# Kernel optimization log

Measured on AMD Instinct MI355X. Metric: run time of the kernel, lower is better.

The kernel has to match this reference:

```python
import jax, jax.numpy as jnp
import numpy as np

B, L = 4, 1024
D_IN, D_MODEL = 2, 512
N_LAYERS, D_STATE, D_CONV, EXPAND, DT_RANK = 2, 16, 4, 2, 32
D_INNER = EXPAND * D_MODEL
EPS = 1e-5


def setup_inputs() -> dict:
    key = jax.random.key(0)
    ks = jax.random.split(key, 10)
    s = 0.02
    return {
        "x": jax.random.normal(ks[0], (B, L, D_IN), jnp.float32),
        "emb_W": jax.random.normal(ks[1], (D_MODEL, D_IN), jnp.float32) * s,
        "emb_b": jnp.zeros((D_MODEL,), jnp.float32),
        "norm_w": jnp.ones((N_LAYERS, D_MODEL), jnp.float32),
        "in_proj_W": jax.random.normal(ks[2], (N_LAYERS, 2 * D_INNER, D_MODEL), jnp.float32) * s,
        "conv_W": jax.random.normal(ks[3], (N_LAYERS, D_INNER, 1, D_CONV), jnp.float32) * s,
        "conv_b": jnp.zeros((N_LAYERS, D_INNER), jnp.float32),
        "x_proj_W": jax.random.normal(ks[4], (N_LAYERS, DT_RANK + 2 * D_STATE, D_INNER), jnp.float32) * s,
        "dt_proj_W": jax.random.normal(ks[5], (N_LAYERS, D_INNER, DT_RANK), jnp.float32) * s,
        "dt_proj_b": jax.random.uniform(ks[6], (N_LAYERS, D_INNER), jnp.float32, -4.0, -2.0),
        "A_log": jnp.log(jnp.broadcast_to(jnp.arange(1, D_STATE + 1, dtype=jnp.float32), (N_LAYERS, D_INNER, D_STATE)) + 0.0),
        "Dskip": jnp.ones((N_LAYERS, D_INNER), jnp.float32),
        "out_proj_W": jax.random.normal(ks[7], (N_LAYERS, D_MODEL, D_INNER), jnp.float32) * s,
        "normf_w": jnp.ones((D_MODEL,), jnp.float32),
    }


def rmsnorm(x, w):
    return x * jax.lax.rsqrt(jnp.mean(x * x, axis=-1, keepdims=True) + EPS) * w


def selective_scan(u, delta, A, Bm, Cm, Dskip):
    # u, delta: (B,L,ED); A: (ED,N); Bm, Cm: (B,L,N); Dskip: (ED,)
    deltaA = jnp.exp(delta[..., None] * A)                      # (B,L,ED,N)
    BX = (delta[..., None] * Bm[:, :, None, :]) * u[..., None]  # (B,L,ED,N)

    def step(h, inp):
        dA, bx, c = inp
        h = dA * h + bx                       # (B,ED,N)
        y = jnp.einsum('ben,bn->be', h, c)    # (B,ED)
        return h, y

    h0 = jnp.zeros((u.shape[0], u.shape[2], A.shape[1]), u.dtype)
    _, ys = jax.lax.scan(step, h0, (deltaA.swapaxes(0, 1), BX.swapaxes(0, 1), Cm.swapaxes(0, 1)))
    y = ys.swapaxes(0, 1)                     # (B,L,ED)
    return y + Dskip * u


def mamba_layer(x, norm_w, ipW, cW, cb, xpW, dtW, dtb, A_log, Dk, opW):
    h = rmsnorm(x, norm_w)
    xz = h @ ipW.T                            # (B,L,2*ED)
    u, z = jnp.split(xz, 2, axis=-1)
    # causal depthwise conv over sequence dim
    uc = jax.lax.conv_general_dilated(
        u.swapaxes(1, 2), cW, window_strides=(1,), padding=[(D_CONV - 1, 0)],
        feature_group_count=D_INNER, dimension_numbers=('NCH', 'OIH', 'NCH'))
    u = jax.nn.silu(uc.swapaxes(1, 2) + cb)   # (B,L,ED)
    xdb = u @ xpW.T                           # (B,L,dt_rank+2N)
    dt, Bm, Cm = jnp.split(xdb, [DT_RANK, DT_RANK + D_STATE], axis=-1)
    delta = jax.nn.softplus(dt @ dtW.T + dtb)
    A = -jnp.exp(A_log)
    y = selective_scan(u, delta, A, Bm, Cm, Dk)
    y = y * jax.nn.silu(z)
    return x + y @ opW.T


def reference(x, emb_W, emb_b, norm_w, in_proj_W, conv_W, conv_b, x_proj_W,
              dt_proj_W, dt_proj_b, A_log, Dskip, out_proj_W, normf_w):
    h = x @ emb_W.T + emb_b                   # (B,L,D_MODEL)
    for l in range(N_LAYERS):
        h = mamba_layer(h, norm_w[l], in_proj_W[l], conv_W[l], conv_b[l],
                        x_proj_W[l], dt_proj_W[l], dt_proj_b[l], A_log[l],
                        Dskip[l], out_proj_W[l])
    return rmsnorm(h, normf_w)
```

## Files before the change

### kernel.cpp

```cpp
#include <hip/hip_runtime.h>
#include <math.h>
#include <stddef.h>

#define BB 4
#define LL 1024
#define DM 512
#define ED 1024
#define NST 16
#define DTR 32
#define XDBC 64
#define BL (BB*LL)
#define CS 16
#define NC 64
#define XKS 16
#define XPAD 68
#define DPAD 132

typedef __attribute__((ext_vector_type(8))) short bf16x8;
typedef __attribute__((ext_vector_type(4))) float f32x4;
typedef unsigned short ushort_t;

__device__ __forceinline__ float silu_f(float x) { return x / (1.f + __expf(-x)); }

__device__ __forceinline__ ushort_t f2b(float f) {
    unsigned int u = __float_as_uint(f);
    unsigned int r = (u + 0x7FFFu + ((u >> 16) & 1u)) >> 16;
    return (ushort_t)r;
}
__device__ __forceinline__ float b2f(ushort_t v) {
    return __uint_as_float(((unsigned int)v) << 16);
}
__device__ __forceinline__ ushort_t f2h(float f) {
    _Float16 h = (_Float16)f;
    return *(ushort_t*)&h;
}
__device__ __forceinline__ float h2f(ushort_t v) {
    _Float16 h = *(_Float16*)&v;
    return (float)h;
}

__device__ __forceinline__ void gload16(const ushort_t* g, ushort_t* l) {
    __builtin_amdgcn_global_load_lds(
        (const __attribute__((address_space(1))) unsigned int*)g,
        (__attribute__((address_space(3))) unsigned int*)l, 16, 0, 0);
}

__global__ void k_embed(const float* __restrict__ x, const float* __restrict__ W,
                        const float* __restrict__ bias, float* __restrict__ h) {
    int i = blockIdx.x * 256 + threadIdx.x;
    if (i >= BL * DM) return;
    int d = i % DM, r = i / DM;
    h[i] = x[r * 2 + 0] * W[d * 2 + 0] + x[r * 2 + 1] * W[d * 2 + 1] + bias[d];
}

__global__ void k_cvt2(const float* __restrict__ ip, const float* __restrict__ op,
                       ushort_t* __restrict__ wip, ushort_t* __restrict__ wop,
                       int n1, int n2) {
    int i = blockIdx.x * 256 + threadIdx.x;
    const float* src; ushort_t* dst; int q;
    if (i < n1) { src = ip; dst = wip; q = i; }
    else if (i < n1 + n2) { src = op; dst = wop; q = i - n1; }
    else return;
    float4 v = *(const float4*)(src + (size_t)q * 4);
    ushort_t o[4] = {f2b(v.x), f2b(v.y), f2b(v.z), f2b(v.w)};
    *(uint2*)(dst + (size_t)q * 4) = *(uint2*)o;
}

template <int BF16OUT>
__global__ __launch_bounds__(256) void k_rmsnorm(const float* __restrict__ in,
                                                 const float* __restrict__ w,
                                                 void* __restrict__ outp) {
    int m = blockIdx.x;
    int tid = threadIdx.x;
    const float* row = in + (size_t)m * DM;
    float2 v = *(const float2*)(row + tid * 2);
    float ss = v.x * v.x + v.y * v.y;
    #pragma unroll
    for (int o = 32; o > 0; o >>= 1) ss += __shfl_down(ss, o, 64);
    __shared__ float red[4];
    int wid = tid >> 6;
    if ((tid & 63) == 0) red[wid] = ss;
    __syncthreads();
    float tot = red[0] + red[1] + red[2] + red[3];
    float rs = rsqrtf(tot * (1.f / DM) + 1e-5f);
    float2 wv = *(const float2*)(w + tid * 2);
    float ox = v.x * rs * wv.x;
    float oy = v.y * rs * wv.y;
    if (BF16OUT) {
        ushort_t o[2] = {f2b(ox), f2b(oy)};
        *(unsigned int*)((ushort_t*)outp + (size_t)m * DM + tid * 2) = *(unsigned int*)o;
    } else {
        *(float2*)((float*)outp + (size_t)m * DM + tid * 2) = make_float2(ox, oy);
    }
}

template <int ADDRES, int BF16OUT, int NT>
__global__ __launch_bounds__(256) void k_bgemm(const ushort_t* __restrict__ A,
                                               const ushort_t* __restrict__ W,
                                               const float* __restrict__ Res,
                                               void* __restrict__ C,
                                               int M, int N, int K, int lda, int ldc) {
    __shared__ ushort_t As[128 * 32];
    __shared__ ushort_t Bs[NT * 32];
    constexpr int NFJ = NT / 32;
    int tid = threadIdx.x;
    int bm = blockIdx.y * 128, bn = blockIdx.x * NT;
    int wave = tid >> 6, lane = tid & 63;
    int wr = wave >> 1, wc = wave & 1;
    int lr = lane & 15;
    int kc = lane >> 4;
    f32x4 acc[4][NFJ];
    #pragma unroll
    for (int i = 0; i < 4; ++i)
        #pragma unroll
        for (int j = 0; j < NFJ; ++j) acc[i][j] = (f32x4){0.f, 0.f, 0.f, 0.f};

    for (int k0 = 0; k0 < K; k0 += 32) {
        __syncthreads();
        #pragma unroll
        for (int ii = 0; ii < 2; ++ii) {
            int g = wave * 128 + ii * 64 + lane;
            int row = g >> 2;
            int c = (g & 3) ^ ((g >> 3) & 3);
            gload16(A + (size_t)(bm + row) * lda + k0 + c * 8,
                    As + (size_t)(wave * 128 + ii * 64) * 8);
        }
        #pragma unroll
        for (int ii = 0; ii < NFJ / 2; ++ii) {
            int g = wave * (NFJ / 2) * 64 + ii * 64 + lane;
            int row = g >> 2;
            int c = (g & 3) ^ ((g >> 3) & 3);
            gload16(W + (size_t)(bn + row) * K + k0 + c * 8,
                    Bs + (size_t)(wave * (NFJ / 2) * 64 + ii * 64) * 8);
        }
        __syncthreads();
        bf16x8 af[4], bfr[NFJ];
        #pragma unroll
        for (int i = 0; i < 4; ++i) {
            int ra = wr * 64 + i * 16 + lr;
            int ca = kc ^ ((ra >> 1) & 3);
            af[i] = *(const bf16x8*)(As + ra * 32 + ca * 8);
        }
        #pragma unroll
        for (int j = 0; j < NFJ; ++j) {
            int rb = wc * (NT / 2) + j * 16 + lr;
            int cb = kc ^ ((rb >> 1) & 3);
            bfr[j] = *(const bf16x8*)(Bs + rb * 32 + cb * 8);
        }
        #pragma unroll
        for (int i = 0; i < 4; ++i)
            #pragma unroll
            for (int j = 0; j < NFJ; ++j)
                acc[i][j] = __builtin_amdgcn_mfma_f32_16x16x32_bf16(af[i], bfr[j], acc[i][j], 0, 0, 0);
    }
    int crow0 = bm + wr * 64 + (lane >> 4) * 4;
    #pragma unroll
    for (int i = 0; i < 4; ++i)
        #pragma unroll
        for (int j = 0; j < NFJ; ++j)
            #pragma unroll
            for (int r = 0; r < 4; ++r) {
                size_t off = (size_t)(crow0 + i * 16 + r) * ldc + bn + wc * (NT / 2) + j * 16 + lr;
                float v = acc[i][j][r];
                if (ADDRES) v += Res[off];
                if (BF16OUT) ((ushort_t*)C)[off] = f2b(v);
                else         ((float*)C)[off] = v;
            }
}

__global__ __launch_bounds__(256) void k_xproj(const ushort_t* __restrict__ A,
                                               const float* __restrict__ W,
                                               float* __restrict__ Pp) {
    __shared__ float As[64][XPAD];
    __shared__ float Ws[64][XPAD];
    int tid = threadIdx.x;
    int k0 = blockIdx.x * 64;
    int bm = blockIdx.y * 64;
    int r = tid >> 2;
    int kc = (tid & 3) * 16;
    const ushort_t* ap = A + (size_t)(bm + r) * ED + k0 + kc;
    const float4* wp = (const float4*)(W + (size_t)r * ED + k0 + kc);
    uint4 a0 = *(const uint4*)(ap);
    uint4 a1 = *(const uint4*)(ap + 8);
    const ushort_t* pa0 = (const ushort_t*)&a0;
    const ushort_t* pa1 = (const ushort_t*)&a1;
    #pragma unroll
    for (int i = 0; i < 8; ++i) {
        As[kc + i][r] = b2f(pa0[i]);
        As[kc + 8 + i][r] = b2f(pa1[i]);
    }
    #pragma unroll
    for (int i = 0; i < 4; ++i) {
        float4 wv = wp[i];
        Ws[kc + i * 4 + 0][r] = wv.x; Ws[kc + i * 4 + 1][r] = wv.y;
        Ws[kc + i * 4 + 2][r] = wv.z; Ws[kc + i * 4 + 3][r] = wv.w;
    }
    __syncthreads();
    int tm = (tid >> 4) * 4;
    int tn = (tid & 15) * 4;
    float acc[4][4] = {};
    #pragma unroll 4
    for (int k = 0; k < 64; ++k) {
        float4 a = *(const float4*)&As[k][tm];
        float4 b = *(const float4*)&Ws[k][tn];
        acc[0][0] += a.x * b.x; acc[0][1] += a.x * b.y; acc[0][2] += a.x * b.z; acc[0][3] += a.x * b.w;
        acc[1][0] += a.y * b.x; acc[1][1] += a.y * b.y; acc[1][2] += a.y * b.z; acc[1][3] += a.y * b.w;
        acc[2][0] += a.z * b.x; acc[2][1] += a.z * b.y; acc[2][2] += a.z * b.z; acc[2][3] += a.z * b.w;
        acc[3][0] += a.w * b.x; acc[3][1] += a.w * b.y; acc[3][2] += a.w * b.z; acc[3][3] += a.w * b.w;
    }
    float* pp = Pp + (size_t)blockIdx.x * BL * XDBC;
    #pragma unroll
    for (int i = 0; i < 4; ++i)
        *(float4*)(pp + (size_t)(bm + tm + i) * XDBC + tn) =
            make_float4(acc[i][0], acc[i][1], acc[i][2], acc[i][3]);
}

__global__ void k_xred(const float* __restrict__ Pp, float* __restrict__ xdb) {
    int i = blockIdx.x * 256 + threadIdx.x;
    float4 s = make_float4(0.f, 0.f, 0.f, 0.f);
    #pragma unroll
    for (int sl = 0; sl < XKS; ++sl) {
        float4 v = *(const float4*)(Pp + (size_t)sl * BL * XDBC + (size_t)i * 4);
        s.x += v.x; s.y += v.y; s.z += v.z; s.w += v.w;
    }
    *(float4*)(xdb + (size_t)i * 4) = s;
}

__global__ void k_conv(const ushort_t* __restrict__ xzb, const float* __restrict__ cw,
                       const float* __restrict__ cb, ushort_t* __restrict__ u) {
    int i = blockIdx.x * 256 + threadIdx.x;
    if (i >= BL * ED) return;
    int e = i % ED;
    int t = (i / ED) % LL;
    int b = i / (ED * LL);
    const ushort_t* col = xzb + (size_t)b * LL * 2048 + e;
    float4 w4 = *(const float4*)(cw + e * 4);
    float acc = cb[e];
    if (t >= 3) acc += b2f(col[(size_t)(t - 3) * 2048]) * w4.x;
    if (t >= 2) acc += b2f(col[(size_t)(t - 2) * 2048]) * w4.y;
    if (t >= 1) acc += b2f(col[(size_t)(t - 1) * 2048]) * w4.z;
    acc += b2f(col[(size_t)t * 2048]) * w4.w;
    u[i] = f2b(silu_f(acc));
}

__global__ __launch_bounds__(256) void k_delta(const float* __restrict__ xdb,
                                               const float* __restrict__ dtW,
                                               const float* __restrict__ dtb,
                                               ushort_t* __restrict__ dyh) {
    __shared__ float Dt[32][DPAD];
    __shared__ float Wt[32][DPAD];
    int tid = threadIdx.x;
    int bm = blockIdx.y * 128;
    int bn = blockIdx.x * 128;
    int r = tid >> 1;
    int hh = (tid & 1) * 16;
    const float4* dp = (const float4*)(xdb + (size_t)(bm + r) * XDBC + hh);
    const float4* wp = (const float4*)(dtW + (size_t)(bn + r) * 32 + hh);
    #pragma unroll
    for (int i = 0; i < 4; ++i) {
        float4 v = dp[i];
        Dt[hh + i * 4 + 0][r] = v.x; Dt[hh + i * 4 + 1][r] = v.y;
        Dt[hh + i * 4 + 2][r] = v.z; Dt[hh + i * 4 + 3][r] = v.w;
        float4 w = wp[i];
        Wt[hh + i * 4 + 0][r] = w.x; Wt[hh + i * 4 + 1][r] = w.y;
        Wt[hh + i * 4 + 2][r] = w.z; Wt[hh + i * 4 + 3][r] = w.w;
    }
    __syncthreads();
    int tm = (tid >> 4) * 8;
    int tn = (tid & 15) * 8;
    float acc[8][8] = {};
    #pragma unroll 8
    for (int k = 0; k < 32; ++k) {
        float4 a0 = *(const float4*)&Dt[k][tm];
        float4 a1 = *(const float4*)&Dt[k][tm + 4];
        float4 b0 = *(const float4*)&Wt[k][tn];
        float4 b1 = *(const float4*)&Wt[k][tn + 4];
        float a[8] = {a0.x, a0.y, a0.z, a0.w, a1.x, a1.y, a1.z, a1.w};
        float b[8] = {b0.x, b0.y, b0.z, b0.w, b1.x, b1.y, b1.z, b1.w};
        #pragma unroll
        for (int i = 0; i < 8; ++i)
            #pragma unroll
            for (int j = 0; j < 8; ++j) acc[i][j] += a[i] * b[j];
    }
    float4 t0 = *(const float4*)(dtb + bn + tn);
    float4 t1 = *(const float4*)(dtb + bn + tn + 4);
    float bias[8] = {t0.x, t0.y, t0.z, t0.w, t1.x, t1.y, t1.z, t1.w};
    #pragma unroll
    for (int i = 0; i < 8; ++i) {
        ushort_t o16[8];
        #pragma unroll
        for (int j = 0; j < 8; ++j) {
            float v = acc[i][j] + bias[j];
            v = (v > 20.f) ? v : __logf(1.f + __expf(v));
            o16[j] = f2h(v);
        }
        size_t off = (size_t)(bm + tm + i) * ED + bn + tn;
        *(uint4*)(dyh + off) = *(uint4*)o16;
    }
}

__global__ __launch_bounds__(256) void k_scan1(const ushort_t* __restrict__ dyh,
                                               const ushort_t* __restrict__ u,
                                               const float* __restrict__ xdb,
                                               const float* __restrict__ A_log,
                                               float* __restrict__ P,
                                               float* __restrict__ S) {
    int tid = threadIdx.x;
    int e = ((blockIdx.x & 3) << 8) + tid;
    int c = (blockIdx.x >> 2) & (NC - 1);
    int b = blockIdx.x >> 8;
    float Ac[16];
    const float4* ap = (const float4*)(A_log + (size_t)e * NST);
    #pragma unroll
    for (int q = 0; q < 4; ++q) {
        float4 a = ap[q];
        Ac[q * 4 + 0] = -__expf(a.x); Ac[q * 4 + 1] = -__expf(a.y);
        Ac[q * 4 + 2] = -__expf(a.z); Ac[q * 4 + 3] = -__expf(a.w);
    }
    float h[16] = {};
    float s = 0.f;
    const ushort_t* dp = dyh + ((size_t)b * LL + c * CS) * ED + e;
    const ushort_t* up = u + ((size_t)b * LL + c * CS) * ED + e;
    const float* xp = xdb + ((size_t)b * LL + c * CS) * XDBC;
    for (int tt = 0; tt < CS; ++tt) {
        float dv = h2f(dp[(size_t)tt * ED]);
        float uv = b2f(up[(size_t)tt * ED]);
        s += dv;
        float du = dv * uv;
        const float4* bp = (const float4*)(xp + tt * XDBC + DTR);
        #pragma unroll
        for (int q = 0; q < 4; ++q) {
            float4 bv = bp[q];
            h[q * 4 + 0] = __expf(dv * Ac[q * 4 + 0]) * h[q * 4 + 0] + du * bv.x;
            h[q * 4 + 1] = __expf(dv * Ac[q * 4 + 1]) * h[q * 4 + 1] + du * bv.y;
            h[q * 4 + 2] = __expf(dv * Ac[q * 4 + 2]) * h[q * 4 + 2] + du * bv.z;
            h[q * 4 + 3] = __expf(dv * Ac[q * 4 + 3]) * h[q * 4 + 3] + du * bv.w;
        }
    }
    float4* pp = (float4*)(P + ((size_t)(b * NC + c) * ED + e) * NST);
    pp[0] = make_float4(h[0], h[1], h[2], h[3]);
    pp[1] = make_float4(h[4], h[5], h[6], h[7]);
    pp[2] = make_float4(h[8], h[9], h[10], h[11]);
    pp[3] = make_float4(h[12], h[13], h[14], h[15]);
    S[(size_t)(b * NC + c) * ED + e] = s;
}

__global__ __launch_bounds__(256) void k_scan2(float* __restrict__ P,
                                               const float* __restrict__ S,
                                               const float* __restrict__ A_log) {
    int i = blockIdx.x * 256 + threadIdx.x;
    int n = i & 15;
    int e = (i >> 4) & (ED - 1);
    int b = i >> 14;
    float Ac = -__expf(A_log[(size_t)e * NST + n]);
    float hin = 0.f;
    for (int c = 0; c < NC; ++c) {
        size_t base = (size_t)(b * NC + c) * ED + e;
        float p = P[base * NST + n];
        float s = S[base];
        P[base * NST + n] = hin;
        hin = __expf(Ac * s) * hin + p;
    }
}

__global__ __launch_bounds__(256) void k_scan3(const ushort_t* __restrict__ dyh,
                                               const ushort_t* __restrict__ u,
                                               const float* __restrict__ xdb,
                                               const ushort_t* __restrict__ xzb,
                                               const float* __restrict__ A_log,
                                               const float* __restrict__ Dskip,
                                               const float* __restrict__ P,
                                               ushort_t* __restrict__ yb) {
    int tid = threadIdx.x;
    int e = ((blockIdx.x & 3) << 8) + tid;
    int c = (blockIdx.x >> 2) & (NC - 1);
    int b = blockIdx.x >> 8;
    float Ac[16], h[16];
    const float4* ap = (const float4*)(A_log + (size_t)e * NST);
    #pragma unroll
    for (int q = 0; q < 4; ++q) {
        float4 a = ap[q];
        Ac[q * 4 + 0] = -__expf(a.x); Ac[q * 4 + 1] = -__expf(a.y);
        Ac[q * 4 + 2] = -__expf(a.z); Ac[q * 4 + 3] = -__expf(a.w);
    }
    const float4* pp = (const float4*)(P + ((size_t)(b * NC + c) * ED + e) * NST);
    #pragma unroll
    for (int q = 0; q < 4; ++q) {
        float4 hv = pp[q];
        h[q * 4 + 0] = hv.x; h[q * 4 + 1] = hv.y;
        h[q * 4 + 2] = hv.z; h[q * 4 + 3] = hv.w;
    }
    float Dk = Dskip[e];
    const ushort_t* dp = dyh + ((size_t)b * LL + c * CS) * ED + e;
    const ushort_t* up = u + ((size_t)b * LL + c * CS) * ED + e;
    const float* xp = xdb + ((size_t)b * LL + c * CS) * XDBC;
    const ushort_t* zp = xzb + ((size_t)b * LL + c * CS) * 2048 + 1024 + e;
    ushort_t* yp = yb + ((size_t)b * LL + c * CS) * ED + e;
    for (int tt = 0; tt < CS; ++tt) {
        float dv = h2f(dp[(size_t)tt * ED]);
        float uv = b2f(up[(size_t)tt * ED]);
        float zv = b2f(zp[(size_t)tt * 2048]);
        float du = dv * uv;
        const float4* bp = (const float4*)(xp + tt * XDBC + DTR);
        const float4* cp = (const float4*)(xp + tt * XDBC + DTR + NST);
        float y = 0.f;
        #pragma unroll
        for (int q = 0; q < 4; ++q) {
            float4 bv = bp[q];
            float4 cv = cp[q];
            h[q * 4 + 0] = __expf(dv * Ac[q * 4 + 0]) * h[q * 4 + 0] + du * bv.x;
            h[q * 4 + 1] = __expf(dv * Ac[q * 4 + 1]) * h[q * 4 + 1] + du * bv.y;
            h[q * 4 + 2] = __expf(dv * Ac[q * 4 + 2]) * h[q * 4 + 2] + du * bv.z;
            h[q * 4 + 3] = __expf(dv * Ac[q * 4 + 3]) * h[q * 4 + 3] + du * bv.w;
            y += h[q * 4 + 0] * cv.x + h[q * 4 + 1] * cv.y +
                 h[q * 4 + 2] * cv.z + h[q * 4 + 3] * cv.w;
        }
        yp[(size_t)tt * ED] = f2b((y + Dk * uv) * silu_f(zv));
    }
}

extern "C" void kernel_launch(void* const* d_in, const int* in_sizes, int n_in,
                              void* d_out, int out_size, void* d_ws, size_t ws_size,
                              hipStream_t stream) {
    const float* x     = (const float*)d_in[0];
    const float* embW  = (const float*)d_in[1];
    const float* embB  = (const float*)d_in[2];
    const float* normw = (const float*)d_in[3];
    const float* ipW   = (const float*)d_in[4];
    const float* cW    = (const float*)d_in[5];
    const float* cb    = (const float*)d_in[6];
    const float* xpW   = (const float*)d_in[7];
    const float* dtW   = (const float*)d_in[8];
    const float* dtb   = (const float*)d_in[9];
    const float* Alog  = (const float*)d_in[10];
    const float* Dsk   = (const float*)d_in[11];
    const float* opW   = (const float*)d_in[12];
    const float* normfw= (const float*)d_in[13];
    float* out = (float*)d_out;

    float* ws  = (float*)d_ws;
    float* h   = ws;
    ushort_t* xzb = (ushort_t*)(h + (size_t)BL * DM);
    ushort_t* ub  = xzb + (size_t)BL * 2 * ED;
    float* xdb = (float*)(ub + (size_t)BL * ED);
    float* Pp  = xdb + (size_t)BL * XDBC;
    float* S   = Pp + (size_t)XKS * BL * XDBC;
    ushort_t* wip = (ushort_t*)(S + (size_t)BB * NC * ED);
    ushort_t* wop = wip + (size_t)2 * 2 * ED * DM;
    ushort_t* yb  = wop + (size_t)2 * DM * ED;
    float* P      = Pp;
    ushort_t* hnb = (ushort_t*)d_out;
    ushort_t* dyh = (ushort_t*)d_out;

    k_embed<<<(BL * DM + 255) / 256, 256, 0, stream>>>(x, embW, embB, h);
    int n1 = 2 * 2 * ED * DM / 4, n2 = 2 * DM * ED / 4;
    k_cvt2<<<(n1 + n2 + 255) / 256, 256, 0, stream>>>(ipW, opW, wip, wop, n1, n2);

    for (int l = 0; l < 2; ++l) {
        const float* Al = Alog + (size_t)l * ED * NST;
        k_rmsnorm<1><<<BL, 256, 0, stream>>>(h, normw + (size_t)l * DM, hnb);
        k_bgemm<0, 1, 128><<<dim3(2 * ED / 128, BL / 128), 256, 0, stream>>>(
            hnb, wip + (size_t)l * 2 * ED * DM, nullptr, xzb, BL, 2 * ED, DM, DM, 2 * ED);
        k_conv<<<(BL * ED + 255) / 256, 256, 0, stream>>>(
            xzb, cW + (size_t)l * ED * 4, cb + (size_t)l * ED, ub);
        k_xproj<<<dim3(XKS, BL / 64), 256, 0, stream>>>(
            ub, xpW + (size_t)l * XDBC * ED, Pp);
        k_xred<<<BL * XDBC / 4 / 256, 256, 0, stream>>>(Pp, xdb);
        k_delta<<<dim3(ED / 128, BL / 128), 256, 0, stream>>>(
            xdb, dtW + (size_t)l * ED * DTR, dtb + (size_t)l * ED, dyh);
        k_scan1<<<BB * NC * (ED / 256), 256, 0, stream>>>(dyh, ub, xdb, Al, P, S);
        k_scan2<<<BB * ED * NST / 256, 256, 0, stream>>>(P, S, Al);
        k_scan3<<<BB * NC * (ED / 256), 256, 0, stream>>>(
            dyh, ub, xdb, xzb, Al, Dsk + (size_t)l * ED, P, yb);
        k_bgemm<1, 0, 64><<<dim3(DM / 64, BL / 128), 256, 0, stream>>>(
            yb, wop + (size_t)l * DM * ED, h, h, BL, DM, ED, ED, DM);
    }
    k_rmsnorm<0><<<BL, 256, 0, stream>>>(h, normfw, out);
}
```

Measured before the change: 297.3 us.

## Fuse conv, x_proj, and dt_proj into one row-tiled mid kernel

Replaces the separate causal-conv, split-K x_proj, reduction, and delta kernels with a single kernel. Each block handles 16 rows: it computes conv+SiLU into shared memory, does the full-K x_proj with a two-way K split reduced in shared memory, then computes dt_proj+softplus from the shared xdb tile. Embedding and weight conversion are also merged into one launch. This removes three launches and the split-K partial buffer round trip. In exchange it uses a scalar FMA GEMM with reloaded x_proj weights per block and only 256 blocks, which may limit parallelism.

```diff
diff --git a/kernel.cpp b/kernel.cpp
--- a/kernel.cpp
+++ b/kernel.cpp
@@ -12,9 +12,7 @@
 #define BL (BB*LL)
 #define CS 16
 #define NC 64
-#define XKS 16
-#define XPAD 68
-#define DPAD 132
+#define MT 16
 
 typedef __attribute__((ext_vector_type(8))) short bf16x8;
 typedef __attribute__((ext_vector_type(4))) float f32x4;
@@ -45,21 +43,21 @@
         (__attribute__((address_space(3))) unsigned int*)l, 16, 0, 0);
 }
 
-__global__ void k_embed(const float* __restrict__ x, const float* __restrict__ W,
-                        const float* __restrict__ bias, float* __restrict__ h) {
+__global__ void k_init(const float* __restrict__ x, const float* __restrict__ embW,
+                       const float* __restrict__ embB, float* __restrict__ h,
+                       const float* __restrict__ ipW, const float* __restrict__ opW,
+                       ushort_t* __restrict__ wip, ushort_t* __restrict__ wop,
+                       int nEmb, int n1, int n2) {
     int i = blockIdx.x * 256 + threadIdx.x;
-    if (i >= BL * DM) return;
-    int d = i % DM, r = i / DM;
-    h[i] = x[r * 2 + 0] * W[d * 2 + 0] + x[r * 2 + 1] * W[d * 2 + 1] + bias[d];
-}
-
-__global__ void k_cvt2(const float* __restrict__ ip, const float* __restrict__ op,
-                       ushort_t* __restrict__ wip, ushort_t* __restrict__ wop,
-                       int n1, int n2) {
-    int i = blockIdx.x * 256 + threadIdx.x;
+    if (i < nEmb) {
+        int d = i % DM, r = i / DM;
+        h[i] = x[r * 2 + 0] * embW[d * 2 + 0] + x[r * 2 + 1] * embW[d * 2 + 1] + embB[d];
+        return;
+    }
+    i -= nEmb;
     const float* src; ushort_t* dst; int q;
-    if (i < n1) { src = ip; dst = wip; q = i; }
-    else if (i < n1 + n2) { src = op; dst = wop; q = i - n1; }
+    if (i < n1) { src = ipW; dst = wip; q = i; }
+    else if (i < n1 + n2) { src = opW; dst = wop; q = i - n1; }
     else return;
     float4 v = *(const float4*)(src + (size_t)q * 4);
     ushort_t o[4] = {f2b(v.x), f2b(v.y), f2b(v.z), f2b(v.w)};
@@ -168,134 +166,122 @@
             }
 }
 
-__global__ __launch_bounds__(256) void k_xproj(const ushort_t* __restrict__ A,
-                                               const float* __restrict__ W,
-                                               float* __restrict__ Pp) {
-    __shared__ float As[64][XPAD];
-    __shared__ float Ws[64][XPAD];
+__global__ __launch_bounds__(512) void k_mid(const ushort_t* __restrict__ xzb,
+                                             const float* __restrict__ cw,
+                                             const float* __restrict__ cb,
+                                             const float* __restrict__ xpW,
+                                             const float* __restrict__ dtW,
+                                             const float* __restrict__ dtb,
+                                             ushort_t* __restrict__ ub,
+                                             float* __restrict__ xdb,
+                                             ushort_t* __restrict__ dyh) {
+    __shared__ ushort_t Ut[MT][1032];
+    __shared__ float Wt[64][68];
+    __shared__ float Xs[MT][68];
+    __shared__ float Xs2[MT][68];
     int tid = threadIdx.x;
-    int k0 = blockIdx.x * 64;
-    int bm = blockIdx.y * 64;
-    int r = tid >> 2;
-    int kc = (tid & 3) * 16;
-    const ushort_t* ap = A + (size_t)(bm + r) * ED + k0 + kc;
-    const float4* wp = (const float4*)(W + (size_t)r * ED + k0 + kc);
-    uint4 a0 = *(const uint4*)(ap);
-    uint4 a1 = *(const uint4*)(ap + 8);
-    const ushort_t* pa0 = (const ushort_t*)&a0;
-    const ushort_t* pa1 = (const ushort_t*)&a1;
-    #pragma unroll
-    for (int i = 0; i < 8; ++i) {
-        As[kc + i][r] = b2f(pa0[i]);
-        As[kc + 8 + i][r] = b2f(pa1[i]);
-    }
-    #pragma unroll
-    for (int i = 0; i < 4; ++i) {
-        float4 wv = wp[i];
-        Ws[kc + i * 4 + 0][r] = wv.x; Ws[kc + i * 4 + 1][r] = wv.y;
-        Ws[kc + i * 4 + 2][r] = wv.z; Ws[kc + i * 4 + 3][r] = wv.w;
+    int bm = blockIdx.x * MT;
+
+    {
+        int e0 = (tid & 255) * 4;
+        int th = (tid >> 8) * 8;
+        float cw4[4][4], cb4[4];
+        #pragma unroll
+        for (int i = 0; i < 4; ++i) {
+            float4 w = *(const float4*)(cw + (size_t)(e0 + i) * 4);
+            cw4[i][0] = w.x; cw4[i][1] = w.y; cw4[i][2] = w.z; cw4[i][3] = w.w;
+        }
+        float4 cbv = *(const float4*)(cb + e0);
+        cb4[0] = cbv.x; cb4[1] = cbv.y; cb4[2] = cbv.z; cb4[3] = cbv.w;
+        #pragma unroll
+        for (int i = 0; i < 8; ++i) {
+            int t = th + i;
+            int row = bm + t;
+            int tloc = row & (LL - 1);
+            const ushort_t* xrow = xzb + (size_t)row * 2048 + e0;
+            uint2 z2 = make_uint2(0, 0);
+            uint2 v3 = *(const uint2*)xrow;
+            uint2 v2 = (tloc >= 1) ? *(const uint2*)(xrow - 2048) : z2;
+            uint2 v1 = (tloc >= 2) ? *(const uint2*)(xrow - 4096) : z2;
+            uint2 v0 = (tloc >= 3) ? *(const uint2*)(xrow - 6144) : z2;
+            const ushort_t* p0 = (const ushort_t*)&v0;
+            const ushort_t* p1 = (const ushort_t*)&v1;
+            const ushort_t* p2 = (const ushort_t*)&v2;
+            const ushort_t* p3 = (const ushort_t*)&v3;
+            ushort_t ures[4];
+            #pragma unroll
+            for (int e = 0; e < 4; ++e) {
+                float a = cb4[e] + b2f(p0[e]) * cw4[e][0] + b2f(p1[e]) * cw4[e][1]
+                                 + b2f(p2[e]) * cw4[e][2] + b2f(p3[e]) * cw4[e][3];
+                ures[e] = f2b(silu_f(a));
+            }
+            *(uint2*)(&Ut[t][e0]) = *(uint2*)ures;
+            *(uint2*)(ub + (size_t)row * ED + e0) = *(uint2*)ures;
+        }
     }
     __syncthreads();
-    int tm = (tid >> 4) * 4;
-    int tn = (tid & 15) * 4;
-    float acc[4][4] = {};
-    #pragma unroll 4
-    for (int k = 0; k < 64; ++k) {
-        float4 a = *(const float4*)&As[k][tm];
-        float4 b = *(const float4*)&Ws[k][tn];
-        acc[0][0] += a.x * b.x; acc[0][1] += a.x * b.y; acc[0][2] += a.x * b.z; acc[0][3] += a.x * b.w;
-        acc[1][0] += a.y * b.x; acc[1][1] += a.y * b.y; acc[1][2] += a.y * b.z; acc[1][3] += a.y * b.w;
-        acc[2][0] += a.z * b.x; acc[2][1] += a.z * b.y; acc[2][2] += a.z * b.z; acc[2][3] += a.z * b.w;
-        acc[3][0] += a.w * b.x; acc[3][1] += a.w * b.y; acc[3][2] += a.w * b.z; acc[3][3] += a.w * b.w;
-    }
-    float* pp = Pp + (size_t)blockIdx.x * BL * XDBC;
-    #pragma unroll
-    for (int i = 0; i < 4; ++i)
-        *(float4*)(pp + (size_t)(bm + tm + i) * XDBC + tn) =
-            make_float4(acc[i][0], acc[i][1], acc[i][2], acc[i][3]);
-}
-
-__global__ void k_xred(const float* __restrict__ Pp, float* __restrict__ xdb) {
-    int i = blockIdx.x * 256 + threadIdx.x;
-    float4 s = make_float4(0.f, 0.f, 0.f, 0.f);
-    #pragma unroll
-    for (int sl = 0; sl < XKS; ++sl) {
-        float4 v = *(const float4*)(Pp + (size_t)sl * BL * XDBC + (size_t)i * 4);
-        s.x += v.x; s.y += v.y; s.z += v.z; s.w += v.w;
-    }
-    *(float4*)(xdb + (size_t)i * 4) = s;
-}
-
-__global__ void k_conv(const ushort_t* __restrict__ xzb, const float* __restrict__ cw,
-                       const float* __restrict__ cb, ushort_t* __restrict__ u) {
-    int i = blockIdx.x * 256 + threadIdx.x;
-    if (i >= BL * ED) return;
-    int e = i % ED;
-    int t = (i / ED) % LL;
-    int b = i / (ED * LL);
-    const ushort_t* col = xzb + (size_t)b * LL * 2048 + e;
-    float4 w4 = *(const float4*)(cw + e * 4);
-    float acc = cb[e];
-    if (t >= 3) acc += b2f(col[(size_t)(t - 3) * 2048]) * w4.x;
-    if (t >= 2) acc += b2f(col[(size_t)(t - 2) * 2048]) * w4.y;
-    if (t >= 1) acc += b2f(col[(size_t)(t - 1) * 2048]) * w4.z;
-    acc += b2f(col[(size_t)t * 2048]) * w4.w;
-    u[i] = f2b(silu_f(acc));
-}
-
-__global__ __launch_bounds__(256) void k_delta(const float* __restrict__ xdb,
-                                               const float* __restrict__ dtW,
-                                               const float* __restrict__ dtb,
-                                               ushort_t* __restrict__ dyh) {
-    __shared__ float Dt[32][DPAD];
-    __shared__ float Wt[32][DPAD];
-    int tid = threadIdx.x;
-    int bm = blockIdx.y * 128;
-    int bn = blockIdx.x * 128;
-    int r = tid >> 1;
-    int hh = (tid & 1) * 16;
-    const float4* dp = (const float4*)(xdb + (size_t)(bm + r) * XDBC + hh);
-    const float4* wp = (const float4*)(dtW + (size_t)(bn + r) * 32 + hh);
-    #pragma unroll
-    for (int i = 0; i < 4; ++i) {
-        float4 v = dp[i];
-        Dt[hh + i * 4 + 0][r] = v.x; Dt[hh + i * 4 + 1][r] = v.y;
-        Dt[hh + i * 4 + 2][r] = v.z; Dt[hh + i * 4 + 3][r] = v.w;
-        float4 w = wp[i];
-        Wt[hh + i * 4 + 0][r] = w.x; Wt[hh + i * 4 + 1][r] = w.y;
-        Wt[hh + i * 4 + 2][r] = w.z; Wt[hh + i * 4 + 3][r] = w.w;
+
+    {
+        int n0 = (tid & 15) * 4;
+        int tg = tid >> 4;
+        int t = tg & 15;
+        int ks = tg >> 4;
+        f32x4 acc = (f32x4){0.f, 0.f, 0.f, 0.f};
+        int wn = tid >> 3, wq = tid & 7;
+        for (int kcn = 0; kcn < 16; ++kcn) {
+            __syncthreads();
+            {
+                const float4* wp = (const float4*)(xpW + (size_t)wn * ED + kcn * 64 + wq * 8);
+                float4 wa = wp[0], wb = wp[1];
+                float wv[8] = {wa.x, wa.y, wa.z, wa.w, wb.x, wb.y, wb.z, wb.w};
+                #pragma unroll
+                for (int r = 0; r < 8; ++r) Wt[wq * 8 + r][wn] = wv[r];
+            }
+            __syncthreads();
+            const ushort_t* urow = &Ut[t][kcn * 64 + ks * 32];
+            #pragma unroll 8
+            for (int j = 0; j < 32; ++j) {
+                float uu = b2f(urow[j]);
+                float4 wv = *(const float4*)&Wt[ks * 32 + j][n0];
+                acc.x += uu * wv.x; acc.y += uu * wv.y;
+                acc.z += uu * wv.z; acc.w += uu * wv.w;
+            }
+        }
+        if (ks == 1) *(f32x4*)&Xs2[t][n0] = acc;
+        __syncthreads();
+        if (ks == 0) {
+            f32x4 o = *(const f32x4*)&Xs2[t][n0];
+            o.x += acc.x; o.y += acc.y; o.z += acc.z; o.w += acc.w;
+            *(f32x4*)&Xs[t][n0] = o;
+            *(float4*)(xdb + (size_t)(bm + t) * XDBC + n0) = make_float4(o.x, o.y, o.z, o.w);
+        }
     }
     __syncthreads();
-    int tm = (tid >> 4) * 8;
-    int tn = (tid & 15) * 8;
-    float acc[8][8] = {};
-    #pragma unroll 8
-    for (int k = 0; k < 32; ++k) {
-        float4 a0 = *(const float4*)&Dt[k][tm];
-        float4 a1 = *(const float4*)&Dt[k][tm + 4];
-        float4 b0 = *(const float4*)&Wt[k][tn];
-        float4 b1 = *(const float4*)&Wt[k][tn + 4];
-        float a[8] = {a0.x, a0.y, a0.z, a0.w, a1.x, a1.y, a1.z, a1.w};
-        float b[8] = {b0.x, b0.y, b0.z, b0.w, b1.x, b1.y, b1.z, b1.w};
-        #pragma unroll
-        for (int i = 0; i < 8; ++i)
+
+    #pragma unroll
+    for (int eh = 0; eh < 2; ++eh) {
+        int e = eh * 512 + tid;
+        float w[32];
+        const float4* wp = (const float4*)(dtW + (size_t)e * DTR);
+        #pragma unroll
+        for (int q = 0; q < 8; ++q) {
+            float4 v = wp[q];
+            w[q * 4 + 0] = v.x; w[q * 4 + 1] = v.y;
+            w[q * 4 + 2] = v.z; w[q * 4 + 3] = v.w;
+        }
+        float bias = dtb[e];
+        #pragma unroll
+        for (int t = 0; t < MT; ++t) {
+            float accv = bias;
             #pragma unroll
-            for (int j = 0; j < 8; ++j) acc[i][j] += a[i] * b[j];
-    }
-    float4 t0 = *(const float4*)(dtb + bn + tn);
-    float4 t1 = *(const float4*)(dtb + bn + tn + 4);
-    float bias[8] = {t0.x, t0.y, t0.z, t0.w, t1.x, t1.y, t1.z, t1.w};
-    #pragma unroll
-    for (int i = 0; i < 8; ++i) {
-        ushort_t o16[8];
-        #pragma unroll
-        for (int j = 0; j < 8; ++j) {
-            float v = acc[i][j] + bias[j];
-            v = (v > 20.f) ? v : __logf(1.f + __expf(v));
-            o16[j] = f2h(v);
-        }
-        size_t off = (size_t)(bm + tm + i) * ED + bn + tn;
-        *(uint4*)(dyh + off) = *(uint4*)o16;
+            for (int q = 0; q < 8; ++q) {
+                float4 d = *(const float4*)&Xs[t][q * 4];
+                accv += d.x * w[q * 4 + 0] + d.y * w[q * 4 + 1] +
+                        d.z * w[q * 4 + 2] + d.w * w[q * 4 + 3];
+            }
+            float dv = (accv > 20.f) ? accv : __logf(1.f + __expf(accv));
+            dyh[(size_t)(bm + t) * ED + e] = f2h(dv);
+        }
     }
 }
 
@@ -443,31 +429,28 @@
     ushort_t* xzb = (ushort_t*)(h + (size_t)BL * DM);
     ushort_t* ub  = xzb + (size_t)BL * 2 * ED;
     float* xdb = (float*)(ub + (size_t)BL * ED);
-    float* Pp  = xdb + (size_t)BL * XDBC;
-    float* S   = Pp + (size_t)XKS * BL * XDBC;
+    float* P   = xdb + (size_t)BL * XDBC;
+    float* S   = P + (size_t)BB * NC * ED * NST;
     ushort_t* wip = (ushort_t*)(S + (size_t)BB * NC * ED);
     ushort_t* wop = wip + (size_t)2 * 2 * ED * DM;
     ushort_t* yb  = wop + (size_t)2 * DM * ED;
-    float* P      = Pp;
     ushort_t* hnb = (ushort_t*)d_out;
     ushort_t* dyh = (ushort_t*)d_out;
 
-    k_embed<<<(BL * DM + 255) / 256, 256, 0, stream>>>(x, embW, embB, h);
+    int nEmb = BL * DM;
     int n1 = 2 * 2 * ED * DM / 4, n2 = 2 * DM * ED / 4;
-    k_cvt2<<<(n1 + n2 + 255) / 256, 256, 0, stream>>>(ipW, opW, wip, wop, n1, n2);
+    k_init<<<(nEmb + n1 + n2 + 255) / 256, 256, 0, stream>>>(
+        x, embW, embB, h, ipW, opW, wip, wop, nEmb, n1, n2);
 
     for (int l = 0; l < 2; ++l) {
         const float* Al = Alog + (size_t)l * ED * NST;
         k_rmsnorm<1><<<BL, 256, 0, stream>>>(h, normw + (size_t)l * DM, hnb);
         k_bgemm<0, 1, 128><<<dim3(2 * ED / 128, BL / 128), 256, 0, stream>>>(
             hnb, wip + (size_t)l * 2 * ED * DM, nullptr, xzb, BL, 2 * ED, DM, DM, 2 * ED);
-        k_conv<<<(BL * ED + 255) / 256, 256, 0, stream>>>(
-            xzb, cW + (size_t)l * ED * 4, cb + (size_t)l * ED, ub);
-        k_xproj<<<dim3(XKS, BL / 64), 256, 0, stream>>>(
-            ub, xpW + (size_t)l * XDBC * ED, Pp);
-        k_xred<<<BL * XDBC / 4 / 256, 256, 0, stream>>>(Pp, xdb);
-        k_delta<<<dim3(ED / 128, BL / 128), 256, 0, stream>>>(
-            xdb, dtW + (size_t)l * ED * DTR, dtb + (size_t)l * ED, dyh);
+        k_mid<<<BL / MT, 512, 0, stream>>>(
+            xzb, cW + (size_t)l * ED * 4, cb + (size_t)l * ED,
+            xpW + (size_t)l * XDBC * ED, dtW + (size_t)l * ED * DTR,
+            dtb + (size_t)l * ED, ub, xdb, dyh);
         k_scan1<<<BB * NC * (ED / 256), 256, 0, stream>>>(dyh, ub, xdb, Al, P, S);
         k_scan2<<<BB * ED * NST / 256, 256, 0, stream>>>(P, S, Al);
         k_scan3<<<BB * NC * (ED / 256), 256, 0, stream>>>(
```

Result: slower. 304.4 us (+2.4%).
